# Optimization experiments

Measured on AMD Instinct MI355X. Metric: run time of the kernel, lower is better.

## Reference

```python
import jax, jax.numpy as jnp
import numpy as np

B, D, H, W, C = 2, 16, 16, 16, 64
CBAR = 32


def setup_inputs() -> dict:
    key = jax.random.key(0)
    ks = jax.random.split(key, 6)
    x = jax.random.normal(ks[0], (B, D, H, W, C), dtype=jnp.float32)
    # 1x1x1 Conv3D == per-voxel linear over channels; scale for stable softmax
    Wf = jax.random.normal(ks[1], (C, CBAR), dtype=jnp.float32) / np.sqrt(C)
    Wg = jax.random.normal(ks[2], (C, CBAR), dtype=jnp.float32) / np.sqrt(C)
    Wh = jax.random.normal(ks[3], (C, CBAR), dtype=jnp.float32) / np.sqrt(C)
    Wo = jax.random.normal(ks[4], (CBAR, C), dtype=jnp.float32) / np.sqrt(CBAR)
    bf = jnp.zeros((CBAR,), jnp.float32)
    bg = jnp.zeros((CBAR,), jnp.float32)
    bh = jnp.zeros((CBAR,), jnp.float32)
    bo = jnp.zeros((C,), jnp.float32)
    gamma = jnp.ones((), jnp.float32)
    return {"x": x, "Wf": Wf, "bf": bf, "Wg": Wg, "bg": bg,
            "Wh": Wh, "bh": bh, "Wo": Wo, "bo": bo, "gamma": gamma}


def reference(x, Wf, bf, Wg, bg, Wh, bh, Wo, bo, gamma):
    b, d, h, w, c = x.shape
    n = d * h * w
    xf = x.reshape(b, n, c)                       # [B, N, C]
    f = xf @ Wf + bf                              # [B, N, cbar] (keys)
    g = xf @ Wg + bg                              # [B, N, cbar] (queries)
    hv = xf @ Wh + bh                             # [B, N, cbar] (values)
    s = jnp.einsum('bqc,bkc->bqk', g, f)          # [B, N, N]
    beta = jax.nn.softmax(s, axis=-1)
    bhv = jnp.einsum('bqk,bkc->bqc', beta, hv)    # [B, N, cbar]
    o = bhv @ Wo + bo                             # [B, N, C]
    out = xf + gamma * o
    return out.reshape(b, d, h, w, c)
```

## Files before the change

kernel.cpp:

```cpp
#include <hip/hip_runtime.h>
#include <hip/hip_bf16.h>

typedef short short8 __attribute__((ext_vector_type(8)));
typedef float f32x4 __attribute__((ext_vector_type(4)));
typedef float f32x2 __attribute__((ext_vector_type(2)));

__device__ __forceinline__ float bf2f(unsigned short v) {
    unsigned int u = ((unsigned int)v) << 16;
    float f;
    __builtin_memcpy(&f, &u, 4);
    return f;
}

__device__ __forceinline__ unsigned short f2bf(float f) {
    unsigned int u;
    __builtin_memcpy(&u, &f, 4);
    u += 0x7fffu + ((u >> 16) & 1u);
    return (unsigned short)(u >> 16);
}

__device__ __forceinline__ unsigned int pack2(float a, float b) {
    return (unsigned int)f2bf(a) | ((unsigned int)f2bf(b) << 16);
}

__device__ __forceinline__ unsigned int pack_trunc(float a, float b) {
    unsigned int ua, ub;
    __builtin_memcpy(&ua, &a, 4);
    __builtin_memcpy(&ub, &b, 4);
    return __builtin_amdgcn_perm(ub, ua, 0x07060302u);
}

__device__ __forceinline__ void split2(float a, float b,
                                       unsigned int& hi, unsigned int& lo) {
    unsigned short ah = f2bf(a), bh = f2bf(b);
    float al = a - bf2f(ah), bl = b - bf2f(bh);
    hi = (unsigned int)ah | ((unsigned int)bh << 16);
    lo = (unsigned int)f2bf(al) | ((unsigned int)f2bf(bl) << 16);
}

__device__ __forceinline__ float loadv(const void* p, int idx, bool is_fp32) {
    return is_fp32 ? ((const float*)p)[idx] : bf2f(((const unsigned short*)p)[idx]);
}
__device__ __forceinline__ bool detect_fp32(const void* x, int tid, int* flag_sh) {
    if (tid < 64) {
        unsigned int w = ((const unsigned int*)x)[tid];
        unsigned int e = (w >> 7) & 0xFFu;
        unsigned long long m = __ballot(e > 140u);
        if (tid == 0) *flag_sh = (__popcll(m) >= 8) ? 1 : 0;
    }
    __syncthreads();
    return *flag_sh != 0;
}

__global__ __launch_bounds__(512) void proj_kernel(
    const void* __restrict__ x,
    const void* __restrict__ Wf, const void* __restrict__ bfv,
    const void* __restrict__ Wg, const void* __restrict__ bgv,
    const void* __restrict__ Wh, const void* __restrict__ bhv,
    unsigned short* __restrict__ F, unsigned short* __restrict__ G,
    unsigned short* __restrict__ Ht) {
    __shared__ unsigned int WTh[3 * 32 * 36];
    __shared__ unsigned int WTl[3 * 32 * 36];
    __shared__ float bL[96];
    __shared__ int dflag;
    int tid = threadIdx.x;
    bool fp32 = detect_fp32(x, tid, &dflag);
    int lane = tid & 63, wave = tid >> 6;
    int Q = lane >> 4, l15 = lane & 15;

    const void* Ws[3] = {Wf, Wg, Wh};
    const void* bs[3] = {bfv, bgv, bhv};

    for (int i = tid; i < 3072; i += 512) {
        int m = i >> 10;
        int r = i & 1023;
        int p = r >> 5, n = r & 31;
        float e0 = loadv(Ws[m], (2 * p) * 32 + n, fp32);
        float e1 = loadv(Ws[m], (2 * p + 1) * 32 + n, fp32);
        unsigned int hi, lo;
        split2(e0, e1, hi, lo);
        WTh[(m * 32 + n) * 36 + p] = hi;
        WTl[(m * 32 + n) * 36 + p] = lo;
    }
    if (tid < 96) bL[tid] = loadv(bs[tid >> 5], tid & 31, fp32);

    int rt = wave >> 2;
    int row0 = (blockIdx.x << 5) + (rt << 4);
    short8 a0h, a0l, a1h, a1l;
    {
        int base = (row0 + l15) * 64 + Q * 8;
        union { unsigned int u[4]; short8 s8; } A0h, A0l, A1h, A1l;
        if (fp32) {
            const float* xf = (const float*)x;
            f32x4 v0 = *(const f32x4*)(xf + base);
            f32x4 v1 = *(const f32x4*)(xf + base + 4);
            f32x4 w0 = *(const f32x4*)(xf + base + 32);
            f32x4 w1 = *(const f32x4*)(xf + base + 36);
            split2(v0[0], v0[1], A0h.u[0], A0l.u[0]);
            split2(v0[2], v0[3], A0h.u[1], A0l.u[1]);
            split2(v1[0], v1[1], A0h.u[2], A0l.u[2]);
            split2(v1[2], v1[3], A0h.u[3], A0l.u[3]);
            split2(w0[0], w0[1], A1h.u[0], A1l.u[0]);
            split2(w0[2], w0[3], A1h.u[1], A1l.u[1]);
            split2(w1[0], w1[1], A1h.u[2], A1l.u[2]);
            split2(w1[2], w1[3], A1h.u[3], A1l.u[3]);
        } else {
            const unsigned short* xb = (const unsigned short*)x;
            A0h.s8 = *(const short8*)(xb + base);
            A1h.s8 = *(const short8*)(xb + base + 32);
            A0l.u[0] = A0l.u[1] = A0l.u[2] = A0l.u[3] = 0;
            A1l = A0l;
        }
        a0h = A0h.s8; a0l = A0l.s8; a1h = A1h.s8; a1l = A1l.s8;
    }
    __syncthreads();

    auto proj_tile = [&](int m, int cb) {
        int rowbase = (m * 32 + cb * 16 + l15) * 36;
        union { uint4 v; short8 s8; } B0h, B0l, B1h, B1l;
        B0h.v = *(const uint4*)&WTh[rowbase + Q * 4];
        B1h.v = *(const uint4*)&WTh[rowbase + 16 + Q * 4];
        B0l.v = *(const uint4*)&WTl[rowbase + Q * 4];
        B1l.v = *(const uint4*)&WTl[rowbase + 16 + Q * 4];
        f32x4 z = {0.f, 0.f, 0.f, 0.f};
        f32x4 acc = __builtin_amdgcn_mfma_f32_16x16x32_bf16(a0h, B0h.s8, z, 0, 0, 0);
        acc = __builtin_amdgcn_mfma_f32_16x16x32_bf16(a0h, B0l.s8, acc, 0, 0, 0);
        acc = __builtin_amdgcn_mfma_f32_16x16x32_bf16(a0l, B0h.s8, acc, 0, 0, 0);
        acc = __builtin_amdgcn_mfma_f32_16x16x32_bf16(a1h, B1h.s8, acc, 0, 0, 0);
        acc = __builtin_amdgcn_mfma_f32_16x16x32_bf16(a1h, B1l.s8, acc, 0, 0, 0);
        acc = __builtin_amdgcn_mfma_f32_16x16x32_bf16(a1l, B1h.s8, acc, 0, 0, 0);
        float bias = bL[m * 32 + cb * 16 + l15];
        if (m < 2) {
            unsigned short* dst = (m == 0) ? F : G;
#pragma unroll
            for (int r = 0; r < 4; r++)
                dst[(row0 + Q * 4 + r) * 32 + cb * 16 + l15] = f2bf(acc[r] + bias);
        } else {
            int bb = row0 >> 12;
            int n0 = (row0 & 4095) + Q * 4;
            uint2 pk;
            pk.x = pack2(acc[0] + bias, acc[1] + bias);
            pk.y = pack2(acc[2] + bias, acc[3] + bias);
            *(uint2*)(Ht + bb * 131072 + (cb * 16 + l15) * 4096 + n0) = pk;
        }
    };
    int c4 = wave & 3;
    proj_tile(c4 >> 1, c4 & 1);
    if (c4 < 2) proj_tile(2, c4);
}

__global__ __launch_bounds__(1024) void attn_kernel(
    const unsigned short* __restrict__ F, const unsigned short* __restrict__ G,
    const unsigned short* __restrict__ Ht,
    const void* __restrict__ x,
    const void* __restrict__ Wo, const void* __restrict__ bo,
    const void* __restrict__ gamma_p,
    void* __restrict__ out) {
    __shared__ __attribute__((aligned(16))) unsigned short P_sh[16][2][16][40];
    __shared__ float O_lds[16][32][32];
    __shared__ float l_lds[16][32];
    __shared__ float Om[32][33];
    __shared__ float lmg[32];
    __shared__ float WoL[32][64];
    __shared__ float boL[64];
    __shared__ int dflag;

    int tid = threadIdx.x;
    bool fp32 = detect_fp32(x, tid, &dflag);

    for (int i = tid; i < 2048; i += 1024) WoL[i >> 6][i & 63] = loadv(Wo, i, fp32);
    if (tid < 64) boL[tid] = loadv(bo, tid, fp32);

    int bx = blockIdx.x;
    int b = bx >> 7;
    int q0 = (bx & 127) << 5;
    int wave = tid >> 6;
    int lane = tid & 63;
    int Q = lane >> 4, l15 = lane & 15;

    const unsigned short* Fb = F + (b << 17);
    const unsigned short* Gb = G + (b << 17);
    const unsigned short* Htb = Ht + (b << 17);

    short8 g0 = *(const short8*)(Gb + ((q0 + l15) << 5) + (Q << 3));
    short8 g1 = *(const short8*)(Gb + ((q0 + 16 + l15) << 5) + (Q << 3));

    f32x4 O00 = {0.f, 0.f, 0.f, 0.f}, O01 = O00, O10 = O00, O11 = O00;
    float ls0 = 0.f, ls1 = 0.f;

    int k_begin = wave << 8;
    short8 af0 = *(const short8*)(Fb + ((k_begin + l15) << 5) + (Q << 3));
    short8 af1 = *(const short8*)(Fb + ((k_begin + 16 + l15) << 5) + (Q << 3));
    short8 bh0 = *(const short8*)(Htb + (l15 << 12) + k_begin + (Q << 3));
    short8 bh1 = *(const short8*)(Htb + ((16 + l15) << 12) + k_begin + (Q << 3));

    for (int it = 0; it < 8; ++it) {
        int itn = (it < 7) ? it + 1 : 7;
        int kn = k_begin + (itn << 5);
        short8 naf0 = *(const short8*)(Fb + ((kn + l15) << 5) + (Q << 3));
        short8 naf1 = *(const short8*)(Fb + ((kn + 16 + l15) << 5) + (Q << 3));
        short8 nbh0 = *(const short8*)(Htb + (l15 << 12) + kn + (Q << 3));
        short8 nbh1 = *(const short8*)(Htb + ((16 + l15) << 12) + kn + (Q << 3));

        f32x4 z = {0.f, 0.f, 0.f, 0.f};
        f32x4 c00 = __builtin_amdgcn_mfma_f32_16x16x32_bf16(af0, g0, z, 0, 0, 0);
        f32x4 c01 = __builtin_amdgcn_mfma_f32_16x16x32_bf16(af1, g0, z, 0, 0, 0);
        f32x4 c10 = __builtin_amdgcn_mfma_f32_16x16x32_bf16(af0, g1, z, 0, 0, 0);
        f32x4 c11 = __builtin_amdgcn_mfma_f32_16x16x32_bf16(af1, g1, z, 0, 0, 0);

        float e00[4], e01[4], e10[4], e11[4];
#pragma unroll
        for (int r = 0; r < 4; r++) {
            e00[r] = __expf(c00[r]); e01[r] = __expf(c01[r]);
            e10[r] = __expf(c10[r]); e11[r] = __expf(c11[r]);
            ls0 += e00[r] + e01[r];
            ls1 += e10[r] + e11[r];
        }

        uint2 w0, w1;
        w0.x = pack_trunc(e00[0], e00[1]); w0.y = pack_trunc(e00[2], e00[3]);
        w1.x = pack_trunc(e01[0], e01[1]); w1.y = pack_trunc(e01[2], e01[3]);
        *(uint2*)&P_sh[wave][0][l15][Q * 4] = w0;
        *(uint2*)&P_sh[wave][0][l15][16 + Q * 4] = w1;
        uint2 w2, w3;
        w2.x = pack_trunc(e10[0], e10[1]); w2.y = pack_trunc(e10[2], e10[3]);
        w3.x = pack_trunc(e11[0], e11[1]); w3.y = pack_trunc(e11[2], e11[3]);
        *(uint2*)&P_sh[wave][1][l15][Q * 4] = w2;
        *(uint2*)&P_sh[wave][1][l15][16 + Q * 4] = w3;

        short8 pf0 = *(const short8*)&P_sh[wave][0][l15][Q * 8];
        short8 pf1 = *(const short8*)&P_sh[wave][1][l15][Q * 8];

        O00 = __builtin_amdgcn_mfma_f32_16x16x32_bf16(pf0, bh0, O00, 0, 0, 0);
        O01 = __builtin_amdgcn_mfma_f32_16x16x32_bf16(pf0, bh1, O01, 0, 0, 0);
        O10 = __builtin_amdgcn_mfma_f32_16x16x32_bf16(pf1, bh0, O10, 0, 0, 0);
        O11 = __builtin_amdgcn_mfma_f32_16x16x32_bf16(pf1, bh1, O11, 0, 0, 0);

        af0 = naf0; af1 = naf1; bh0 = nbh0; bh1 = nbh1;
    }

    ls0 += __shfl_xor(ls0, 16); ls0 += __shfl_xor(ls0, 32);
    ls1 += __shfl_xor(ls1, 16); ls1 += __shfl_xor(ls1, 32);
    if (Q == 0) {
        l_lds[wave][l15] = ls0;
        l_lds[wave][16 + l15] = ls1;
    }
#pragma unroll
    for (int r = 0; r < 4; r++) {
        O_lds[wave][(Q << 2) | r][l15]             = O00[r];
        O_lds[wave][(Q << 2) | r][16 + l15]        = O01[r];
        O_lds[wave][16 + ((Q << 2) | r)][l15]      = O10[r];
        O_lds[wave][16 + ((Q << 2) | r)][16 + l15] = O11[r];
    }
    __syncthreads();

    if (tid < 32) {
        float s = 0.f;
#pragma unroll
        for (int w = 0; w < 16; w++) s += l_lds[w][tid];
        lmg[tid] = 1.0f / s;
    }
    {
        int q = tid >> 5, c = tid & 31;
        float s = 0.f;
#pragma unroll
        for (int w = 0; w < 16; w++) s += O_lds[w][q][c];
        Om[q][c] = s;
    }
    __syncthreads();

    int q = tid >> 5;
    int ch = (tid & 31) << 1;
    float a0 = 0.f, a1 = 0.f;
#pragma unroll
    for (int c = 0; c < 32; c++) {
        float ob = Om[q][c];
        f32x2 wr = *(const f32x2*)&WoL[c][ch];
        a0 += ob * wr[0]; a1 += ob * wr[1];
    }
    float inv = lmg[q];
    float gam = loadv(gamma_p, 0, fp32);
    int gq = q0 + q;
    int obase = (((b << 12) + gq) << 6) + ch;
    if (fp32) {
        f32x2 xv = *(const f32x2*)((const float*)x + obase);
        f32x2 ov;
        ov[0] = xv[0] + gam * (a0 * inv + boL[ch + 0]);
        ov[1] = xv[1] + gam * (a1 * inv + boL[ch + 1]);
        *(f32x2*)((float*)out + obase) = ov;
    } else {
        const unsigned short* xb = (const unsigned short*)x;
        unsigned short* ob16 = (unsigned short*)out;
        unsigned int pk = pack2(bf2f(xb[obase + 0]) + gam * (a0 * inv + boL[ch + 0]),
                                bf2f(xb[obase + 1]) + gam * (a1 * inv + boL[ch + 1]));
        *(unsigned int*)(ob16 + obase) = pk;
    }
}

extern "C" void kernel_launch(void* const* d_in, const int* in_sizes, int n_in,
                              void* d_out, int out_size, void* d_ws, size_t ws_size,
                              hipStream_t stream) {
    const void* x   = d_in[0];
    const void* Wf  = d_in[1];
    const void* bfv = d_in[2];
    const void* Wg  = d_in[3];
    const void* bgv = d_in[4];
    const void* Wh  = d_in[5];
    const void* bhv = d_in[6];
    const void* Wo  = d_in[7];
    const void* bo  = d_in[8];
    const void* gam = d_in[9];

    unsigned short* F  = (unsigned short*)d_ws;
    unsigned short* G  = F + 262144;
    unsigned short* Ht = G + 262144;

    proj_kernel<<<256, 512, 0, stream>>>(x, Wf, bfv, Wg, bgv, Wh, bhv, F, G, Ht);
    attn_kernel<<<256, 1024, 0, stream>>>(F, G, Ht, x, Wo, bo, gam, d_out);
}
```

Before: 93.92 us.

## Software-pipeline P·V MFMA one iteration behind with double-buffered P in LDS

```diff
diff --git a/kernel.cpp b/kernel.cpp
--- a/kernel.cpp
+++ b/kernel.cpp
@@ -156,9 +156,14 @@
     const void* __restrict__ Wo, const void* __restrict__ bo,
     const void* __restrict__ gamma_p,
     void* __restrict__ out) {
-    __shared__ __attribute__((aligned(16))) unsigned short P_sh[16][2][16][40];
-    __shared__ float O_lds[16][32][32];
-    __shared__ float l_lds[16][32];
+    struct PhaseA {
+        unsigned short P[16][2][2][16][40];
+    };
+    struct PhaseB {
+        float O[16][32][32];
+        float l[16][32];
+    };
+    __shared__ __attribute__((aligned(16))) union { PhaseA a; PhaseB b; } U;
     __shared__ float Om[32][33];
     __shared__ float lmg[32];
     __shared__ float WoL[32][64];
@@ -194,7 +199,12 @@
     short8 bh0 = *(const short8*)(Htb + (l15 << 12) + k_begin + (Q << 3));
     short8 bh1 = *(const short8*)(Htb + ((16 + l15) << 12) + k_begin + (Q << 3));
 
+    short8 pf0 = {}, pf1 = {};
+    short8 obh0 = {}, obh1 = {};
+
+#pragma unroll 2
     for (int it = 0; it < 8; ++it) {
+        int buf = it & 1;
         int itn = (it < 7) ? it + 1 : 7;
         int kn = k_begin + (itn << 5);
         short8 naf0 = *(const short8*)(Fb + ((kn + l15) << 5) + (Q << 3));
@@ -220,51 +230,61 @@
         uint2 w0, w1;
         w0.x = pack_trunc(e00[0], e00[1]); w0.y = pack_trunc(e00[2], e00[3]);
         w1.x = pack_trunc(e01[0], e01[1]); w1.y = pack_trunc(e01[2], e01[3]);
-        *(uint2*)&P_sh[wave][0][l15][Q * 4] = w0;
-        *(uint2*)&P_sh[wave][0][l15][16 + Q * 4] = w1;
+        *(uint2*)&U.a.P[wave][buf][0][l15][Q * 4] = w0;
+        *(uint2*)&U.a.P[wave][buf][0][l15][16 + Q * 4] = w1;
         uint2 w2, w3;
         w2.x = pack_trunc(e10[0], e10[1]); w2.y = pack_trunc(e10[2], e10[3]);
         w3.x = pack_trunc(e11[0], e11[1]); w3.y = pack_trunc(e11[2], e11[3]);
-        *(uint2*)&P_sh[wave][1][l15][Q * 4] = w2;
-        *(uint2*)&P_sh[wave][1][l15][16 + Q * 4] = w3;
-
-        short8 pf0 = *(const short8*)&P_sh[wave][0][l15][Q * 8];
-        short8 pf1 = *(const short8*)&P_sh[wave][1][l15][Q * 8];
-
-        O00 = __builtin_amdgcn_mfma_f32_16x16x32_bf16(pf0, bh0, O00, 0, 0, 0);
-        O01 = __builtin_amdgcn_mfma_f32_16x16x32_bf16(pf0, bh1, O01, 0, 0, 0);
-        O10 = __builtin_amdgcn_mfma_f32_16x16x32_bf16(pf1, bh0, O10, 0, 0, 0);
-        O11 = __builtin_amdgcn_mfma_f32_16x16x32_bf16(pf1, bh1, O11, 0, 0, 0);
-
+        *(uint2*)&U.a.P[wave][buf][1][l15][Q * 4] = w2;
+        *(uint2*)&U.a.P[wave][buf][1][l15][16 + Q * 4] = w3;
+
+        if (it > 0) {
+            O00 = __builtin_amdgcn_mfma_f32_16x16x32_bf16(pf0, obh0, O00, 0, 0, 0);
+            O01 = __builtin_amdgcn_mfma_f32_16x16x32_bf16(pf0, obh1, O01, 0, 0, 0);
+            O10 = __builtin_amdgcn_mfma_f32_16x16x32_bf16(pf1, obh0, O10, 0, 0, 0);
+            O11 = __builtin_amdgcn_mfma_f32_16x16x32_bf16(pf1, obh1, O11, 0, 0, 0);
+        }
+
+        pf0 = *(const short8*)&U.a.P[wave][buf][0][l15][Q * 8];
+        pf1 = *(const short8*)&U.a.P[wave][buf][1][l15][Q * 8];
+
+        obh0 = bh0; obh1 = bh1;
         af0 = naf0; af1 = naf1; bh0 = nbh0; bh1 = nbh1;
     }
+    O00 = __builtin_amdgcn_mfma_f32_16x16x32_bf16(pf0, obh0, O00, 0, 0, 0);
+    O01 = __builtin_amdgcn_mfma_f32_16x16x32_bf16(pf0, obh1, O01, 0, 0, 0);
+    O10 = __builtin_amdgcn_mfma_f32_16x16x32_bf16(pf1, obh0, O10, 0, 0, 0);
+    O11 = __builtin_amdgcn_mfma_f32_16x16x32_bf16(pf1, obh1, O11, 0, 0, 0);
 
     ls0 += __shfl_xor(ls0, 16); ls0 += __shfl_xor(ls0, 32);
     ls1 += __shfl_xor(ls1, 16); ls1 += __shfl_xor(ls1, 32);
+
+    __syncthreads();
+
     if (Q == 0) {
-        l_lds[wave][l15] = ls0;
-        l_lds[wave][16 + l15] = ls1;
+        U.b.l[wave][l15] = ls0;
+        U.b.l[wave][16 + l15] = ls1;
     }
 #pragma unroll
     for (int r = 0; r < 4; r++) {
-        O_lds[wave][(Q << 2) | r][l15]             = O00[r];
-        O_lds[wave][(Q << 2) | r][16 + l15]        = O01[r];
-        O_lds[wave][16 + ((Q << 2) | r)][l15]      = O10[r];
-        O_lds[wave][16 + ((Q << 2) | r)][16 + l15] = O11[r];
+        U.b.O[wave][(Q << 2) | r][l15]             = O00[r];
+        U.b.O[wave][(Q << 2) | r][16 + l15]        = O01[r];
+        U.b.O[wave][16 + ((Q << 2) | r)][l15]      = O10[r];
+        U.b.O[wave][16 + ((Q << 2) | r)][16 + l15] = O11[r];
     }
     __syncthreads();
 
     if (tid < 32) {
         float s = 0.f;
 #pragma unroll
-        for (int w = 0; w < 16; w++) s += l_lds[w][tid];
+        for (int w = 0; w < 16; w++) s += U.b.l[w][tid];
         lmg[tid] = 1.0f / s;
     }
     {
         int q = tid >> 5, c = tid & 31;
         float s = 0.f;
 #pragma unroll
-        for (int w = 0; w < 16; w++) s += O_lds[w][q][c];
+        for (int w = 0; w < 16; w++) s += U.b.O[w][q][c];
         Om[q][c] = s;
     }
     __syncthreads();
```

New measurement: 95.91 us. +2.1%, slower.
